# Kernel tuning notes

Hardware: AMD Instinct MI355X
Metric: run time of the kernel (lower is better)

The kernel has to match this reference:

```python
import jax, jax.numpy as jnp
import numpy as np

N = 10000
F_IN = 512
HID = 256
C = 16
N_POST_ITER = 4


def setup_inputs() -> dict:
    key = jax.random.key(0)
    ks = jax.random.split(key, 10)
    raw_adj = jax.random.uniform(ks[0], (N, N), dtype=jnp.float32) * 0.01
    A = jax.random.uniform(ks[1], (N, N), dtype=jnp.float32)
    normed_adj = A / jnp.sum(A, axis=1, keepdims=True)  # row-sum-one normalized
    features = jax.random.normal(ks[2], (N, F_IN), dtype=jnp.float32)
    labels = jax.random.randint(ks[3], (N,), 0, C)
    y_onehot = jax.nn.one_hot(labels, C, dtype=jnp.float32)
    train_mask = jax.random.randint(ks[4], (N,), 0, 2).astype(jnp.bool_)
    # GCN belief estimator params (glorot-ish scaling)
    W1 = jax.random.normal(ks[5], (F_IN, HID), dtype=jnp.float32) / np.sqrt(F_IN)
    b1 = jnp.zeros((HID,), dtype=jnp.float32)
    W2 = jax.random.normal(ks[6], (HID, C), dtype=jnp.float32) / np.sqrt(HID)
    b2 = jnp.zeros((C,), dtype=jnp.float32)
    # class-compatibility matrix H (initialized, zero-centered as in init_H)
    H = jax.random.normal(ks[7], (C, C), dtype=jnp.float32) * 0.1
    return {"raw_adj": raw_adj, "normed_adj": normed_adj, "features": features,
            "y_onehot": y_onehot, "train_mask": train_mask,
            "W1": W1, "b1": b1, "W2": W2, "b2": b2, "H": H}


def reference(raw_adj, normed_adj, features, y_onehot, train_mask, W1, b1, W2, b2, H):
    num_class = y_onehot.shape[1]
    # 2-layer GCN belief estimator: adj @ (x @ W) + b
    h = jax.nn.relu(normed_adj @ (features @ W1) + b1)          # [N, HID]
    logits = normed_adj @ (h @ W2) + b2                          # [N, C]
    # post_process: iterative compatibility-guided belief propagation
    prior_belief = jax.nn.softmax(logits, axis=1)
    E_hat = prior_belief - 1.0 / num_class
    B_hat = E_hat
    for _ in range(N_POST_ITER):
        B_hat = E_hat + raw_adj @ (B_hat @ H)
    post_belief = B_hat + 1.0 / num_class
    return post_belief
```

## Files before the change

kernel.cpp:

```cpp
#include <hip/hip_runtime.h>
#include <hip/hip_bf16.h>

#define NN 10000
#define KP 10048
static constexpr float INV_C = 1.0f / 16.0f;

typedef __attribute__((ext_vector_type(8))) short bf16x8;
typedef __attribute__((ext_vector_type(4))) float f32x4;
typedef unsigned short u16;
typedef unsigned int u32;

__device__ __forceinline__ u16 f2b(float f) {
    return __builtin_bit_cast(u16, __float2bfloat16(f));
}
__device__ __forceinline__ float b2f(u16 b) {
    union { u32 u; float f; } v; v.u = ((u32)b) << 16;
    return v.f;
}
__device__ __forceinline__ bf16x8 pack8(f32x4 a, f32x4 b) {
    bf16x8 o;
    o[0]=f2b(a[0]); o[1]=f2b(a[1]); o[2]=f2b(a[2]); o[3]=f2b(a[3]);
    o[4]=f2b(b[0]); o[5]=f2b(b[1]); o[6]=f2b(b[2]); o[7]=f2b(b[3]);
    return o;
}

#define AS1(p) ((__attribute__((address_space(1))) void*)(p))
#define AS3(p) ((__attribute__((address_space(3))) void*)(p))

__global__ __launch_bounds__(256)
void cvt_feat(const float* __restrict__ src, u16* __restrict__ dst)
{
    int c = blockIdx.x * 256 + threadIdx.x;
    size_t base = (size_t)c * 8;
    f32x4 a = *(const f32x4*)(src + base);
    f32x4 b = *(const f32x4*)(src + base + 4);
    *(bf16x8*)(dst + base) = pack8(a, b);
}

__global__ __launch_bounds__(256)
void w12t(const float* __restrict__ W1, const float* __restrict__ W2,
          float* __restrict__ W1T, u16* __restrict__ W2T)
{
    int bid = blockIdx.x, t = threadIdx.x;
    if (bid < 512) {
        int idx = bid * 256 + t;
        int n = idx >> 9, k = idx & 511;
        W1T[idx] = W1[(size_t)k * 256 + n];
    } else {
        int idx = (bid - 512) * 256 + t;
        if (idx < 4096) {
            int n_ = idx >> 8, k_ = idx & 255;
            W2T[idx] = f2b(W2[(size_t)k_ * 16 + n_]);
        }
    }
}

template<int BIAS, int RELU>
__global__ __launch_bounds__(256)
void gemm_a32_bt16(const float* __restrict__ A, int lda, int M, int Ka,
                   const u16* __restrict__ BT, int ldb, int N, int npad,
                   const float* __restrict__ bias,
                   u16* __restrict__ C, int ldc, int K)
{
    __shared__ u16 Asm[64 * 64];
    __shared__ u16 Bsm[256 * 64];
    const int t = threadIdx.x;
    const int lane = t & 63;
    const int w = t >> 6;
    const int row0 = blockIdx.x * 64;
    const int n0 = blockIdx.y * 256;

    const f32x4 fz = {0.f, 0.f, 0.f, 0.f};
    f32x4 acc[4][4];
#pragma unroll
    for (int i = 0; i < 4; ++i)
#pragma unroll
        for (int j = 0; j < 4; ++j) acc[i][j] = fz;

    const int ar = t >> 2, akq = t & 3;
    int agr = row0 + ar; if (agr > M - 1) agr = M - 1;
    const float* asrc = A + (size_t)agr * lda + akq * 16;
    const int aslot0 = (akq * 2) ^ (ar & 7);
    const int aslot1 = (akq * 2 + 1) ^ (ar & 7);
    const int l8 = lane >> 3, sl = lane & 7;

    for (int k0 = 0; k0 < K; k0 += 64) {
        bool aval = (k0 + akq * 16) < Ka;
        f32x4 x0, x1, x2, x3;
        if (aval) {
            x0 = *(const f32x4*)(asrc + k0);
            x1 = *(const f32x4*)(asrc + k0 + 4);
            x2 = *(const f32x4*)(asrc + k0 + 8);
            x3 = *(const f32x4*)(asrc + k0 + 12);
        } else {
            x0 = x1 = x2 = x3 = fz;
        }
#pragma unroll
        for (int i = 0; i < 8; ++i) {
            int lr = i * 32 + w * 8 + l8;
            int gn = n0 + lr; if (gn > N - 1) gn = N - 1;
            int ss = sl ^ (lr & 7);
            const u16* src = BT + (size_t)gn * ldb + k0 + ss * 8;
            __builtin_amdgcn_global_load_lds(AS1(src), AS3(&Bsm[(i * 32 + w * 8) * 64]),
                                             16, 0, 0);
        }
        *(bf16x8*)&Asm[ar * 64 + aslot0 * 8] = pack8(x0, x1);
        *(bf16x8*)&Asm[ar * 64 + aslot1 * 8] = pack8(x2, x3);
        __syncthreads();
#pragma unroll
        for (int kk = 0; kk < 2; ++kk) {
            bf16x8 afr[4], bfr[4];
#pragma unroll
            for (int mi = 0; mi < 4; ++mi) {
                int r = mi * 16 + (lane & 15);
                int s2 = (kk * 4 + (lane >> 4)) ^ (r & 7);
                afr[mi] = *(const bf16x8*)&Asm[r * 64 + s2 * 8];
            }
#pragma unroll
            for (int ni = 0; ni < 4; ++ni) {
                int nr = w * 64 + ni * 16 + (lane & 15);
                int s2 = (kk * 4 + (lane >> 4)) ^ (nr & 7);
                bfr[ni] = *(const bf16x8*)&Bsm[nr * 64 + s2 * 8];
            }
#pragma unroll
            for (int mi = 0; mi < 4; ++mi)
#pragma unroll
                for (int ni = 0; ni < 4; ++ni)
                    acc[mi][ni] = __builtin_amdgcn_mfma_f32_16x16x32_bf16(
                        afr[mi], bfr[ni], acc[mi][ni], 0, 0, 0);
        }
        __syncthreads();
    }
#pragma unroll
    for (int mi = 0; mi < 4; ++mi) {
        int grb = row0 + mi * 16 + (lane >> 4) * 4;
#pragma unroll
        for (int ni = 0; ni < 4; ++ni) {
            int gc = n0 + w * 64 + ni * 16 + (lane & 15);
            if (gc < npad) {
                float bv = (BIAS && gc < N) ? bias[gc] : 0.f;
#pragma unroll
                for (int rg = 0; rg < 4; ++rg) {
                    int gr = grb + rg;
                    if (gr < M) {
                        float v = acc[mi][ni][rg] + bv;
                        if (RELU) v = fmaxf(v, 0.f);
                        C[(size_t)gr * ldc + gc] = f2b(gc < N ? v : 0.f);
                    }
                }
            }
        }
    }
}

__global__ __launch_bounds__(256)
void gemm_na(const float* __restrict__ A, const u16* __restrict__ BT,
             u16* __restrict__ Pws)
{
    __shared__ u16 Asm[64 * 64];
    __shared__ u16 Bsm[256 * 64];
    const int t = threadIdx.x;
    const int lane = t & 63;
    const int w = t >> 6;
    const int row0 = blockIdx.x * 64;
    const int s = blockIdx.y;
    const int c0 = (157 * s) >> 4, c1 = (157 * (s + 1)) >> 4;

    const f32x4 fz = {0.f, 0.f, 0.f, 0.f};
    f32x4 acc[4][4];
#pragma unroll
    for (int i = 0; i < 4; ++i)
#pragma unroll
        for (int j = 0; j < 4; ++j) acc[i][j] = fz;

    const int ar = t >> 2, akq = t & 3;
    const int grow = row0 + ar;
    const int agr = grow < NN ? grow : NN - 1;
    const float* asrc = A + (size_t)agr * NN + akq * 16;
    const int aslot0 = (akq * 2) ^ (ar & 7);
    const int aslot1 = (akq * 2 + 1) ^ (ar & 7);
    const int l8 = lane >> 3, sl = lane & 7;

    f32x4 x0, x1, x2, x3;
    {
        const int k0 = c0 * 64;
        if (k0 + akq * 16 < NN) {
            x0 = *(const f32x4*)(asrc + k0);
            x1 = *(const f32x4*)(asrc + k0 + 4);
            x2 = *(const f32x4*)(asrc + k0 + 8);
            x3 = *(const f32x4*)(asrc + k0 + 12);
        } else {
            x0 = x1 = x2 = x3 = fz;
        }
    }

    for (int ck = c0; ck < c1; ++ck) {
        const int k0 = ck * 64;
#pragma unroll
        for (int i = 0; i < 8; ++i) {
            int lr = i * 32 + w * 8 + l8;
            int ss = sl ^ (lr & 7);
            const u16* src = BT + (size_t)lr * KP + k0 + ss * 8;
            __builtin_amdgcn_global_load_lds(AS1(src), AS3(&Bsm[(i * 32 + w * 8) * 64]),
                                             16, 0, 0);
        }
        *(bf16x8*)&Asm[ar * 64 + aslot0 * 8] = pack8(x0, x1);
        *(bf16x8*)&Asm[ar * 64 + aslot1 * 8] = pack8(x2, x3);
        __syncthreads();
        {
            const int kn = k0 + 64;
            if (ck + 1 < c1 && (kn + akq * 16) < NN) {
                x0 = *(const f32x4*)(asrc + kn);
                x1 = *(const f32x4*)(asrc + kn + 4);
                x2 = *(const f32x4*)(asrc + kn + 8);
                x3 = *(const f32x4*)(asrc + kn + 12);
            } else {
                x0 = x1 = x2 = x3 = fz;
            }
        }
#pragma unroll
        for (int kk = 0; kk < 2; ++kk) {
            bf16x8 afr[4], bfr[4];
#pragma unroll
            for (int mi = 0; mi < 4; ++mi) {
                int r = mi * 16 + (lane & 15);
                int s2 = (kk * 4 + (lane >> 4)) ^ (r & 7);
                afr[mi] = *(const bf16x8*)&Asm[r * 64 + s2 * 8];
            }
#pragma unroll
            for (int ni = 0; ni < 4; ++ni) {
                int nr = w * 64 + ni * 16 + (lane & 15);
                int s2 = (kk * 4 + (lane >> 4)) ^ (nr & 7);
                bfr[ni] = *(const bf16x8*)&Bsm[nr * 64 + s2 * 8];
            }
#pragma unroll
            for (int mi = 0; mi < 4; ++mi)
#pragma unroll
                for (int ni = 0; ni < 4; ++ni)
                    acc[mi][ni] = __builtin_amdgcn_mfma_f32_16x16x32_bf16(
                        afr[mi], bfr[ni], acc[mi][ni], 0, 0, 0);
        }
        __syncthreads();
    }
    u16* outp = Pws + (size_t)s * NN * 256;
#pragma unroll
    for (int mi = 0; mi < 4; ++mi) {
        int grb = row0 + mi * 16 + (lane >> 4) * 4;
#pragma unroll
        for (int ni = 0; ni < 4; ++ni) {
            int gc = w * 64 + ni * 16 + (lane & 15);
#pragma unroll
            for (int rg = 0; rg < 4; ++rg) {
                int gr = grb + rg;
                if (gr < NN)
                    outp[(size_t)gr * 256 + gc] = f2b(acc[mi][ni][rg]);
            }
        }
    }
}

__global__ __launch_bounds__(256)
void reduce_h(const u16* __restrict__ Pws, const float* __restrict__ b1,
              u16* __restrict__ hbf)
{
    int i8 = blockIdx.x * 256 + threadIdx.x;
    size_t base = (size_t)i8 * 8;
    int col = (int)(base & 255);
    float v[8];
#pragma unroll
    for (int j = 0; j < 8; ++j) v[j] = b1[col + j];
#pragma unroll
    for (int s = 0; s < 16; ++s) {
        bf16x8 p = *(const bf16x8*)(Pws + (size_t)s * NN * 256 + base);
#pragma unroll
        for (int j = 0; j < 8; ++j) v[j] += b2f((u16)p[j]);
    }
    bf16x8 o;
#pragma unroll
    for (int j = 0; j < 8; ++j) o[j] = f2b(fmaxf(v[j], 0.f));
    *(bf16x8*)(hbf + base) = o;
}

template<int AFP32, int CVT>
__global__ __launch_bounds__(256)
void adj16(const void* __restrict__ Av, long lda,
           const u16* __restrict__ BT,
           float* __restrict__ Pout, int nch, int nchf,
           u16* __restrict__ Acvt)
{
    const int t = threadIdx.x, lane = t & 63, w = t >> 6;
    const int s = blockIdx.y;
    const int rowu = blockIdx.x * 64 + w * 16 + (lane & 15);
    const int row = rowu < NN ? rowu : NN - 1;
    const int kq = (lane >> 4) * 8;
    const u16* brow = BT + (size_t)(lane & 15) * KP + kq;
    const float* a32 = (const float*)Av + (size_t)row * lda + kq;
    const u16*  a16 = (const u16*) Av + (size_t)row * lda + kq;
    u16* cvtp = CVT ? (Acvt + (size_t)rowu * KP + kq) : (u16*)0;
    const bool wok = CVT && (rowu < NN);

    int c0 = (nch * s) >> 3, c1 = (nch * (s + 1)) >> 3;
    int c1f = c1 < nchf ? c1 : nchf;
    f32x4 acc0 = {0.f, 0.f, 0.f, 0.f};
    f32x4 acc1 = {0.f, 0.f, 0.f, 0.f};
    int kc = c0;
    for (; kc + 4 <= c1f; kc += 4) {
        bf16x8 a[4], b[4];
#pragma unroll
        for (int u = 0; u < 4; ++u) {
            if (AFP32) {
                f32x4 x = *(const f32x4*)(a32 + (size_t)(kc + u) * 32);
                f32x4 y = *(const f32x4*)(a32 + (size_t)(kc + u) * 32 + 4);
                a[u] = pack8(x, y);
            } else {
                a[u] = *(const bf16x8*)(a16 + (size_t)(kc + u) * 32);
            }
            b[u] = *(const bf16x8*)(brow + (size_t)(kc + u) * 32);
        }
        if (CVT && wok) {
#pragma unroll
            for (int u = 0; u < 4; ++u)
                *(bf16x8*)(cvtp + (size_t)(kc + u) * 32) = a[u];
        }
        acc0 = __builtin_amdgcn_mfma_f32_16x16x32_bf16(a[0], b[0], acc0, 0, 0, 0);
        acc1 = __builtin_amdgcn_mfma_f32_16x16x32_bf16(a[1], b[1], acc1, 0, 0, 0);
        acc0 = __builtin_amdgcn_mfma_f32_16x16x32_bf16(a[2], b[2], acc0, 0, 0, 0);
        acc1 = __builtin_amdgcn_mfma_f32_16x16x32_bf16(a[3], b[3], acc1, 0, 0, 0);
    }
    for (; kc < c1; ++kc) {
        bf16x8 a = bf16x8{0,0,0,0,0,0,0,0};
        if (AFP32) {
            if (kc * 32 + kq < NN) {
                f32x4 x = *(const f32x4*)(a32 + (size_t)kc * 32);
                f32x4 y = *(const f32x4*)(a32 + (size_t)kc * 32 + 4);
                a = pack8(x, y);
            }
        } else {
            a = *(const bf16x8*)(a16 + (size_t)kc * 32);
        }
        if (CVT && wok)
            *(bf16x8*)(cvtp + (size_t)kc * 32) = a;
        bf16x8 b = *(const bf16x8*)(brow + (size_t)kc * 32);
        acc0 = __builtin_amdgcn_mfma_f32_16x16x32_bf16(a, b, acc0, 0, 0, 0);
    }
    int ob = blockIdx.x * 64 + w * 16 + (lane >> 4) * 4;
#pragma unroll
    for (int rg = 0; rg < 4; ++rg) {
        int orow = ob + rg;
        if (orow < NN)
            Pout[(size_t)s * (NN * 16) + (size_t)orow * 16 + (lane & 15)] =
                acc0[rg] + acc1[rg];
    }
}

__global__ __launch_bounds__(256)
void hw2_mfma(const u16* __restrict__ h, const u16* __restrict__ W2T,
              u16* __restrict__ outT)
{
    const int t = threadIdx.x, lane = t & 63, w = t >> 6;
    int row = blockIdx.x * 64 + w * 16 + (lane & 15);
    int rowc = row < NN ? row : NN - 1;
    const int kq = (lane >> 4) * 8;
    const u16* arow = h + (size_t)rowc * 256 + kq;
    const u16* brow = W2T + (size_t)(lane & 15) * 256 + kq;
    f32x4 acc = {0.f, 0.f, 0.f, 0.f};
#pragma unroll
    for (int kc = 0; kc < 8; ++kc) {
        bf16x8 a = *(const bf16x8*)(arow + kc * 32);
        bf16x8 b = *(const bf16x8*)(brow + kc * 32);
        acc = __builtin_amdgcn_mfma_f32_16x16x32_bf16(a, b, acc, 0, 0, 0);
    }
    int ob = blockIdx.x * 64 + w * 16 + (lane >> 4) * 4;
    int col = lane & 15;
#pragma unroll
    for (int rg = 0; rg < 4; ++rg) {
        int r = ob + rg;
        outT[(size_t)col * KP + r] = f2b(r < NN ? acc[rg] : 0.f);
    }
}

__global__ __launch_bounds__(256)
void softmax_e_h2(const float* __restrict__ P, const float* __restrict__ b2,
                  const float* __restrict__ H, float* __restrict__ E,
                  u16* __restrict__ bhT)
{
    __shared__ float Hs[256];
    const int t = threadIdx.x;
    Hs[t] = H[t];
    __syncthreads();
    const int l = t & 63, w = t >> 6;
    const int g = l >> 2, sub = l & 3;
    const int row = blockIdx.x * 64 + w * 16 + g;
    const bool valid = row < NN;
    float acc[16];
#pragma unroll
    for (int k = 0; k < 16; ++k) acc[k] = 0.f;
    if (valid) {
        const float* p0 = P + (size_t)(sub * 2) * (NN * 16) + (size_t)row * 16;
        const float* p1 = p0 + (size_t)NN * 16;
#pragma unroll
        for (int q = 0; q < 4; ++q) {
            f32x4 a = *(const f32x4*)(p0 + q * 4);
            f32x4 c = *(const f32x4*)(p1 + q * 4);
#pragma unroll
            for (int j = 0; j < 4; ++j) acc[q * 4 + j] = a[j] + c[j];
        }
        if (sub == 0) {
#pragma unroll
            for (int k = 0; k < 16; ++k) acc[k] += b2[k];
        }
    }
#pragma unroll
    for (int m = 1; m <= 2; m <<= 1)
#pragma unroll
        for (int k = 0; k < 16; ++k) acc[k] += __shfl_xor(acc[k], m, 4);
    float e[16];
    if (valid) {
        float mx = acc[0];
#pragma unroll
        for (int k = 1; k < 16; ++k) mx = fmaxf(mx, acc[k]);
        float ssum = 0.f;
#pragma unroll
        for (int k = 0; k < 16; ++k) { e[k] = __expf(acc[k] - mx); ssum += e[k]; }
        float inv = 1.f / ssum;
#pragma unroll
        for (int k = 0; k < 16; ++k) e[k] = e[k] * inv - INV_C;
        f32x4 eq = {e[sub*4+0], e[sub*4+1], e[sub*4+2], e[sub*4+3]};
        *(f32x4*)(E + (size_t)row * 16 + sub * 4) = eq;
    } else {
#pragma unroll
        for (int k = 0; k < 16; ++k) e[k] = 0.f;
    }
    float o[4] = {0.f, 0.f, 0.f, 0.f};
#pragma unroll
    for (int m2 = 0; m2 < 16; ++m2) {
        float x = e[m2];
#pragma unroll
        for (int j = 0; j < 4; ++j) o[j] += x * Hs[m2 * 16 + sub * 4 + j];
    }
#pragma unroll
    for (int j = 0; j < 4; ++j)
        bhT[(size_t)(sub * 4 + j) * KP + row] = f2b(o[j]);
}

template<int LAST>
__global__ __launch_bounds__(256)
void combine_bmm2(const float* __restrict__ E, const float* __restrict__ P,
                  const float* __restrict__ H, u16* __restrict__ bhT,
                  float* __restrict__ out)
{
    __shared__ float Hs[256];
    const int t = threadIdx.x;
    Hs[t] = H[t];
    __syncthreads();
    const int l = t & 63, w = t >> 6;
    const int g = l >> 2, sub = l & 3;
    const int row = blockIdx.x * 64 + w * 16 + g;
    const bool valid = row < NN;
    float acc[16];
#pragma unroll
    for (int k = 0; k < 16; ++k) acc[k] = 0.f;
    if (valid) {
        const float* p0 = P + (size_t)(sub * 2) * (NN * 16) + (size_t)row * 16;
        const float* p1 = p0 + (size_t)NN * 16;
#pragma unroll
        for (int q = 0; q < 4; ++q) {
            f32x4 a = *(const f32x4*)(p0 + q * 4);
            f32x4 c = *(const f32x4*)(p1 + q * 4);
#pragma unroll
            for (int j = 0; j < 4; ++j) acc[q * 4 + j] = a[j] + c[j];
        }
        if (sub == 0) {
            const float* ep = E + (size_t)row * 16;
#pragma unroll
            for (int k = 0; k < 16; ++k) acc[k] += ep[k];
        }
    }
#pragma unroll
    for (int m = 1; m <= 2; m <<= 1)
#pragma unroll
        for (int k = 0; k < 16; ++k) acc[k] += __shfl_xor(acc[k], m, 4);
    if (LAST) {
        if (valid) {
            f32x4 oq = {acc[sub*4+0] + INV_C, acc[sub*4+1] + INV_C,
                        acc[sub*4+2] + INV_C, acc[sub*4+3] + INV_C};
            *(f32x4*)(out + (size_t)row * 16 + sub * 4) = oq;
        }
    } else {
        if (!valid) {
#pragma unroll
            for (int k = 0; k < 16; ++k) acc[k] = 0.f;
        }
        float o[4] = {0.f, 0.f, 0.f, 0.f};
#pragma unroll
        for (int m2 = 0; m2 < 16; ++m2) {
            float x = acc[m2];
#pragma unroll
            for (int j = 0; j < 4; ++j) o[j] += x * Hs[m2 * 16 + sub * 4 + j];
        }
#pragma unroll
        for (int j = 0; j < 4; ++j)
            bhT[(size_t)(sub * 4 + j) * KP + row] = f2b(o[j]);
    }
}

extern "C" void kernel_launch(void* const* d_in, const int* in_sizes, int n_in,
                              void* d_out, int out_size, void* d_ws, size_t ws_size,
                              hipStream_t stream)
{
    const float* raw_adj    = (const float*)d_in[0];
    const float* normed_adj = (const float*)d_in[1];
    const float* features   = (const float*)d_in[2];
    const float* W1 = (const float*)d_in[5];
    const float* b1 = (const float*)d_in[6];
    const float* W2 = (const float*)d_in[7];
    const float* b2 = (const float*)d_in[8];
    const float* H  = (const float*)d_in[9];
    float* out = (float*)d_out;

    char* ws = (char*)d_ws;
    u16*   featbf = (u16*)  (ws + 0);
    float* P      = (float*)(ws + 0);
    float* E      = (float*)(ws + 5120000);
    float* W1T    = (float*)(ws + 10240000);
    u16*   W2T    = (u16*)  (ws + 10764288);
    u16*   XWT    = (u16*)  (ws + 10772480);
    u16*   hbf    = (u16*)  (ws + 15917056);
    u16*   hw2T   = (u16*)  (ws + 21037056);
    u16*   bhT    = (u16*)  (ws + 21358592);
    const bool mid = ws_size >= (size_t)222640128;
    const bool low = ws_size >= (size_t)103600128;
    u16* Pws  = (u16*)(ws + 21680128);
    u16* ArBf = (u16*)(ws + 21680128);

    cvt_feat<<<2500, 256, 0, stream>>>(features, featbf);
    w12t<<<528, 256, 0, stream>>>(W1, W2, W1T, W2T);

    gemm_a32_bt16<0, 0><<<dim3(4, 40), 256, 0, stream>>>(
        W1T, 512, 256, 512, featbf, 512, NN, KP, nullptr, XWT, KP, 512);

    if (low) {
        gemm_na<<<dim3(157, 16), 256, 0, stream>>>(normed_adj, XWT, Pws);
        reduce_h<<<1250, 256, 0, stream>>>(Pws, b1, hbf);
    } else {
        gemm_a32_bt16<1, 1><<<dim3(157, 1), 256, 0, stream>>>(
            normed_adj, NN, NN, NN, XWT, KP, 256, 256, b1, hbf, 256, KP);
    }

    hw2_mfma<<<157, 256, 0, stream>>>(hbf, W2T, hw2T);

    adj16<1, 0><<<dim3(157, 8), 256, 0, stream>>>(
        (const void*)normed_adj, NN, hw2T, P, 313, 312, nullptr);

    softmax_e_h2<<<157, 256, 0, stream>>>(P, b2, H, E, bhT);

    for (int it = 0; it < 4; ++it) {
        if (mid) {
            if (it == 0)
                adj16<1, 1><<<dim3(157, 8), 256, 0, stream>>>(
                    (const void*)raw_adj, NN, bhT, P, 314, 312, ArBf);
            else
                adj16<0, 0><<<dim3(157, 8), 256, 0, stream>>>(
                    (const void*)ArBf, KP, bhT, P, 314, 314, nullptr);
        } else {
            adj16<1, 0><<<dim3(157, 8), 256, 0, stream>>>(
                (const void*)raw_adj, NN, bhT, P, 313, 312, nullptr);
        }
        if (it == 3)
            combine_bmm2<1><<<157, 256, 0, stream>>>(E, P, H, nullptr, out);
        else
            combine_bmm2<0><<<157, 256, 0, stream>>>(E, P, H, bhT, nullptr);
    }
}
```

Baseline: 591.9 us.

## Double-buffer LDS tiles in gemm_na to overlap loads with MFMA

Converts the A and B shared-memory tiles of the adjacency GEMM into double buffers. The next chunk's B tile is issued via global_load_lds and the next A tile is converted and stored into the alternate buffer before computing on the current one, with register prefetch moved two chunks ahead. This removes one barrier per iteration and hides global-load latency behind MFMA work, at the cost of doubling LDS use (about 80KB per block), which may reduce occupancy.

```diff
diff --git a/kernel.cpp b/kernel.cpp
--- a/kernel.cpp
+++ b/kernel.cpp
@@ -157,8 +157,8 @@
 void gemm_na(const float* __restrict__ A, const u16* __restrict__ BT,
              u16* __restrict__ Pws)
 {
-    __shared__ u16 Asm[64 * 64];
-    __shared__ u16 Bsm[256 * 64];
+    __shared__ u16 Asm[2][64 * 64];
+    __shared__ u16 Bsm[2][256 * 64];
     const int t = threadIdx.x;
     const int lane = t & 63;
     const int w = t >> 6;
@@ -181,9 +181,17 @@
     const int aslot1 = (akq * 2 + 1) ^ (ar & 7);
     const int l8 = lane >> 3, sl = lane & 7;
 
-    f32x4 x0, x1, x2, x3;
     {
         const int k0 = c0 * 64;
+#pragma unroll
+        for (int i = 0; i < 8; ++i) {
+            int lr = i * 32 + w * 8 + l8;
+            int ss = sl ^ (lr & 7);
+            const u16* src = BT + (size_t)lr * KP + k0 + ss * 8;
+            __builtin_amdgcn_global_load_lds(AS1(src),
+                AS3(&Bsm[0][(i * 32 + w * 8) * 64]), 16, 0, 0);
+        }
+        f32x4 x0, x1, x2, x3;
         if (k0 + akq * 16 < NN) {
             x0 = *(const f32x4*)(asrc + k0);
             x1 = *(const f32x4*)(asrc + k0 + 4);
@@ -192,30 +200,46 @@
         } else {
             x0 = x1 = x2 = x3 = fz;
         }
-    }
-
+        *(bf16x8*)&Asm[0][ar * 64 + aslot0 * 8] = pack8(x0, x1);
+        *(bf16x8*)&Asm[0][ar * 64 + aslot1 * 8] = pack8(x2, x3);
+    }
+    f32x4 y0, y1, y2, y3;
+    {
+        const int kn = (c0 + 1) * 64;
+        if (c0 + 1 < c1 && kn + akq * 16 < NN) {
+            y0 = *(const f32x4*)(asrc + kn);
+            y1 = *(const f32x4*)(asrc + kn + 4);
+            y2 = *(const f32x4*)(asrc + kn + 8);
+            y3 = *(const f32x4*)(asrc + kn + 12);
+        } else {
+            y0 = y1 = y2 = y3 = fz;
+        }
+    }
+    __syncthreads();
+
+    int buf = 0;
     for (int ck = c0; ck < c1; ++ck) {
-        const int k0 = ck * 64;
-#pragma unroll
-        for (int i = 0; i < 8; ++i) {
-            int lr = i * 32 + w * 8 + l8;
-            int ss = sl ^ (lr & 7);
-            const u16* src = BT + (size_t)lr * KP + k0 + ss * 8;
-            __builtin_amdgcn_global_load_lds(AS1(src), AS3(&Bsm[(i * 32 + w * 8) * 64]),
-                                             16, 0, 0);
-        }
-        *(bf16x8*)&Asm[ar * 64 + aslot0 * 8] = pack8(x0, x1);
-        *(bf16x8*)&Asm[ar * 64 + aslot1 * 8] = pack8(x2, x3);
-        __syncthreads();
-        {
-            const int kn = k0 + 64;
-            if (ck + 1 < c1 && (kn + akq * 16) < NN) {
-                x0 = *(const f32x4*)(asrc + kn);
-                x1 = *(const f32x4*)(asrc + kn + 4);
-                x2 = *(const f32x4*)(asrc + kn + 8);
-                x3 = *(const f32x4*)(asrc + kn + 12);
+        const int nb = buf ^ 1;
+        if (ck + 1 < c1) {
+            const int kn = (ck + 1) * 64;
+#pragma unroll
+            for (int i = 0; i < 8; ++i) {
+                int lr = i * 32 + w * 8 + l8;
+                int ss = sl ^ (lr & 7);
+                const u16* src = BT + (size_t)lr * KP + kn + ss * 8;
+                __builtin_amdgcn_global_load_lds(AS1(src),
+                    AS3(&Bsm[nb][(i * 32 + w * 8) * 64]), 16, 0, 0);
+            }
+            *(bf16x8*)&Asm[nb][ar * 64 + aslot0 * 8] = pack8(y0, y1);
+            *(bf16x8*)&Asm[nb][ar * 64 + aslot1 * 8] = pack8(y2, y3);
+            const int kf = (ck + 2) * 64;
+            if (ck + 2 < c1 && kf + akq * 16 < NN) {
+                y0 = *(const f32x4*)(asrc + kf);
+                y1 = *(const f32x4*)(asrc + kf + 4);
+                y2 = *(const f32x4*)(asrc + kf + 8);
+                y3 = *(const f32x4*)(asrc + kf + 12);
             } else {
-                x0 = x1 = x2 = x3 = fz;
+                y0 = y1 = y2 = y3 = fz;
             }
         }
 #pragma unroll
@@ -225,13 +249,13 @@
             for (int mi = 0; mi < 4; ++mi) {
                 int r = mi * 16 + (lane & 15);
                 int s2 = (kk * 4 + (lane >> 4)) ^ (r & 7);
-                afr[mi] = *(const bf16x8*)&Asm[r * 64 + s2 * 8];
+                afr[mi] = *(const bf16x8*)&Asm[buf][r * 64 + s2 * 8];
             }
 #pragma unroll
             for (int ni = 0; ni < 4; ++ni) {
                 int nr = w * 64 + ni * 16 + (lane & 15);
                 int s2 = (kk * 4 + (lane >> 4)) ^ (nr & 7);
-                bfr[ni] = *(const bf16x8*)&Bsm[nr * 64 + s2 * 8];
+                bfr[ni] = *(const bf16x8*)&Bsm[buf][nr * 64 + s2 * 8];
             }
 #pragma unroll
             for (int mi = 0; mi < 4; ++mi)
@@ -241,6 +265,7 @@
                         afr[mi], bfr[ni], acc[mi][ni], 0, 0, 0);
         }
         __syncthreads();
+        buf = nb;
     }
     u16* outp = Pws + (size_t)s * NN * 256;
 #pragma unroll
```

New measurement: 598.1 us. Within noise of the previous version (+1.1%).

## Retile normed_adj GEMM to 32-row blocks with 3-way K split

Applied to the files above, without the earlier changes.

Restructures the first adjacency GEMM from 64x256 tiles with a 16-way K split to 32x256 tiles with 512-thread blocks and K step 32, using only a 3-way K split. This cuts the bf16 partial-sum workspace traffic and the reduce_h work, which now sums 3 partials instead of 16. It also lowers the workspace threshold so this path runs on smaller workspaces. In exchange each block computes less per K step, B tiles are reused less across rows, and only half the threads stage A.

```diff
diff --git a/kernel.cpp b/kernel.cpp
--- a/kernel.cpp
+++ b/kernel.cpp
@@ -6,6 +6,7 @@
 static constexpr float INV_C = 1.0f / 16.0f;
 
 typedef __attribute__((ext_vector_type(8))) short bf16x8;
+typedef __attribute__((ext_vector_type(4))) short bf16x4;
 typedef __attribute__((ext_vector_type(4))) float f32x4;
 typedef unsigned short u16;
 typedef unsigned int u32;
@@ -21,6 +22,11 @@
     bf16x8 o;
     o[0]=f2b(a[0]); o[1]=f2b(a[1]); o[2]=f2b(a[2]); o[3]=f2b(a[3]);
     o[4]=f2b(b[0]); o[5]=f2b(b[1]); o[6]=f2b(b[2]); o[7]=f2b(b[3]);
+    return o;
+}
+__device__ __forceinline__ bf16x4 pack4(f32x4 a) {
+    bf16x4 o;
+    o[0]=f2b(a[0]); o[1]=f2b(a[1]); o[2]=f2b(a[2]); o[3]=f2b(a[3]);
     return o;
 }
 
@@ -153,90 +159,83 @@
     }
 }
 
-__global__ __launch_bounds__(256)
+__global__ __launch_bounds__(512, 8)
 void gemm_na(const float* __restrict__ A, const u16* __restrict__ BT,
              u16* __restrict__ Pws)
 {
-    __shared__ u16 Asm[64 * 64];
-    __shared__ u16 Bsm[256 * 64];
+    __shared__ u16 Asm[32 * 32];
+    __shared__ u16 Bsm[256 * 32];
     const int t = threadIdx.x;
     const int lane = t & 63;
     const int w = t >> 6;
-    const int row0 = blockIdx.x * 64;
+    const int row0 = blockIdx.x * 32;
     const int s = blockIdx.y;
-    const int c0 = (157 * s) >> 4, c1 = (157 * (s + 1)) >> 4;
+    const int c0 = (314 * s) / 3, c1 = (314 * (s + 1)) / 3;
 
     const f32x4 fz = {0.f, 0.f, 0.f, 0.f};
-    f32x4 acc[4][4];
-#pragma unroll
-    for (int i = 0; i < 4; ++i)
-#pragma unroll
-        for (int j = 0; j < 4; ++j) acc[i][j] = fz;
-
-    const int ar = t >> 2, akq = t & 3;
-    const int grow = row0 + ar;
+    f32x4 acc[2][2];
+#pragma unroll
+    for (int i = 0; i < 2; ++i)
+#pragma unroll
+        for (int j = 0; j < 2; ++j) acc[i][j] = fz;
+
+    const bool astage = t < 256;
+    const int arow = t >> 3;
+    const int aseg = t & 7;
+    const int grow = row0 + (arow & 31);
     const int agr = grow < NN ? grow : NN - 1;
-    const float* asrc = A + (size_t)agr * NN + akq * 16;
-    const int aslot0 = (akq * 2) ^ (ar & 7);
-    const int aslot1 = (akq * 2 + 1) ^ (ar & 7);
-    const int l8 = lane >> 3, sl = lane & 7;
-
-    f32x4 x0, x1, x2, x3;
+    const float* asrc = A + (size_t)agr * NN + aseg * 4;
+    const int asl = (aseg >> 1) ^ (arow & 3);
+    const int aoff = arow * 32 + asl * 8 + (aseg & 1) * 4;
+
+    const int blr0 = t >> 2;
+    const int bsl = t & 3;
+
+    f32x4 x = fz;
     {
-        const int k0 = c0 * 64;
-        if (k0 + akq * 16 < NN) {
-            x0 = *(const f32x4*)(asrc + k0);
-            x1 = *(const f32x4*)(asrc + k0 + 4);
-            x2 = *(const f32x4*)(asrc + k0 + 8);
-            x3 = *(const f32x4*)(asrc + k0 + 12);
-        } else {
-            x0 = x1 = x2 = x3 = fz;
-        }
+        const int k = c0 * 32 + aseg * 4;
+        if (astage && k + 4 <= NN) x = *(const f32x4*)(asrc + c0 * 32);
     }
 
     for (int ck = c0; ck < c1; ++ck) {
-        const int k0 = ck * 64;
-#pragma unroll
-        for (int i = 0; i < 8; ++i) {
-            int lr = i * 32 + w * 8 + l8;
-            int ss = sl ^ (lr & 7);
+        const int k0 = ck * 32;
+#pragma unroll
+        for (int i = 0; i < 2; ++i) {
+            int lr = i * 128 + blr0;
+            int ss = bsl ^ (lr & 3);
             const u16* src = BT + (size_t)lr * KP + k0 + ss * 8;
-            __builtin_amdgcn_global_load_lds(AS1(src), AS3(&Bsm[(i * 32 + w * 8) * 64]),
-                                             16, 0, 0);
-        }
-        *(bf16x8*)&Asm[ar * 64 + aslot0 * 8] = pack8(x0, x1);
-        *(bf16x8*)&Asm[ar * 64 + aslot1 * 8] = pack8(x2, x3);
+            __builtin_amdgcn_global_load_lds(AS1(src),
+                AS3(&Bsm[(i * 128 + (w << 4)) * 32]), 16, 0, 0);
+        }
+        if (astage)
+            *(bf16x4*)&Asm[aoff] = pack4(x);
         __syncthreads();
         {
-            const int kn = k0 + 64;
-            if (ck + 1 < c1 && (kn + akq * 16) < NN) {
-                x0 = *(const f32x4*)(asrc + kn);
-                x1 = *(const f32x4*)(asrc + kn + 4);
-                x2 = *(const f32x4*)(asrc + kn + 8);
-                x3 = *(const f32x4*)(asrc + kn + 12);
-            } else {
-                x0 = x1 = x2 = x3 = fz;
-            }
-        }
-#pragma unroll
-        for (int kk = 0; kk < 2; ++kk) {
-            bf16x8 afr[4], bfr[4];
-#pragma unroll
-            for (int mi = 0; mi < 4; ++mi) {
+            const int kn = k0 + 32;
+            const int k = kn + aseg * 4;
+            if (astage && ck + 1 < c1 && k + 4 <= NN)
+                x = *(const f32x4*)(asrc + kn);
+            else
+                x = fz;
+        }
+        {
+            bf16x8 afr[2], bfr[2];
+#pragma unroll
+            for (int mi = 0; mi < 2; ++mi) {
                 int r = mi * 16 + (lane & 15);
-                int s2 = (kk * 4 + (lane >> 4)) ^ (r & 7);
-                afr[mi] = *(const bf16x8*)&Asm[r * 64 + s2 * 8];
-            }
-#pragma unroll
-            for (int ni = 0; ni < 4; ++ni) {
-                int nr = w * 64 + ni * 16 + (lane & 15);
-                int s2 = (kk * 4 + (lane >> 4)) ^ (nr & 7);
-                bfr[ni] = *(const bf16x8*)&Bsm[nr * 64 + s2 * 8];
-            }
-#pragma unroll
-            for (int mi = 0; mi < 4; ++mi)
-#pragma unroll
-                for (int ni = 0; ni < 4; ++ni)
+                int s2 = (lane >> 4) ^ (r & 3);
+                afr[mi] = *(const bf16x8*)&Asm[r * 32 + s2 * 8];
+            }
+#pragma unroll
+            for (int ni = 0; ni < 2; ++ni) {
+                int nr = w * 32 + ni * 16 + (lane & 15);
+                int s2 = (lane >> 4) ^ (nr & 3);
+                bfr[ni] = *(const bf16x8*)&Bsm[nr * 32 + s2 * 8];
+            }
+#pragma unroll
+            for (int mi = 0; mi < 2; ++mi)
+#pragma unroll
+                for (int ni = 0; ni < 2; ++ni)
                     acc[mi][ni] = __builtin_amdgcn_mfma_f32_16x16x32_bf16(
                         afr[mi], bfr[ni], acc[mi][ni], 0, 0, 0);
         }
@@ -244,11 +243,11 @@
     }
     u16* outp = Pws + (size_t)s * NN * 256;
 #pragma unroll
-    for (int mi = 0; mi < 4; ++mi) {
+    for (int mi = 0; mi < 2; ++mi) {
         int grb = row0 + mi * 16 + (lane >> 4) * 4;
 #pragma unroll
-        for (int ni = 0; ni < 4; ++ni) {
-            int gc = w * 64 + ni * 16 + (lane & 15);
+        for (int ni = 0; ni < 2; ++ni) {
+            int gc = w * 32 + ni * 16 + (lane & 15);
 #pragma unroll
             for (int rg = 0; rg < 4; ++rg) {
                 int gr = grb + rg;
@@ -259,6 +258,7 @@
     }
 }
 
+template<int NS>
 __global__ __launch_bounds__(256)
 void reduce_h(const u16* __restrict__ Pws, const float* __restrict__ b1,
               u16* __restrict__ hbf)
@@ -270,7 +270,7 @@
 #pragma unroll
     for (int j = 0; j < 8; ++j) v[j] = b1[col + j];
 #pragma unroll
-    for (int s = 0; s < 16; ++s) {
+    for (int s = 0; s < NS; ++s) {
         bf16x8 p = *(const bf16x8*)(Pws + (size_t)s * NN * 256 + base);
 #pragma unroll
         for (int j = 0; j < 8; ++j) v[j] += b2f((u16)p[j]);
@@ -529,7 +529,7 @@
     u16*   hw2T   = (u16*)  (ws + 21037056);
     u16*   bhT    = (u16*)  (ws + 21358592);
     const bool mid = ws_size >= (size_t)222640128;
-    const bool low = ws_size >= (size_t)103600128;
+    const bool low = ws_size >= (size_t)37040128;
     u16* Pws  = (u16*)(ws + 21680128);
     u16* ArBf = (u16*)(ws + 21680128);
 
@@ -540,8 +540,8 @@
         W1T, 512, 256, 512, featbf, 512, NN, KP, nullptr, XWT, KP, 512);
 
     if (low) {
-        gemm_na<<<dim3(157, 16), 256, 0, stream>>>(normed_adj, XWT, Pws);
-        reduce_h<<<1250, 256, 0, stream>>>(Pws, b1, hbf);
+        gemm_na<<<dim3(313, 3), 512, 0, stream>>>(normed_adj, XWT, Pws);
+        reduce_h<3><<<1250, 256, 0, stream>>>(Pws, b1, hbf);
     } else {
         gemm_a32_bt16<1, 1><<<dim3(157, 1), 256, 0, stream>>>(
             normed_adj, NN, NN, NN, XWT, KP, 256, 256, b1, hbf, 256, KP);
```

Result: slower. 657.8 us (+11.1%).
